# Kernel tuning notes

Hardware: AMD Instinct MI355X
Metric: run time of the kernel (lower is better)

## Reference

```python
import jax, jax.numpy as jnp
import numpy as np


def setup_inputs() -> dict:
    key = jax.random.key(0)
    k1, k2 = jax.random.split(key)
    B, F = 256, 512
    mu_in = jax.random.normal(k1, (B, F), dtype=jnp.float32)
    Sigma_in = jax.random.normal(k2, (B, F, F), dtype=jnp.float32)
    return {"mu_in": mu_in, "Sigma_in": Sigma_in}


def reference(mu_in, Sigma_in):
    # mu_out = softmax(mu_in, axis=1)
    p = jax.nn.softmax(mu_in, axis=1)  # [B, F]
    # Per-sample softmax Jacobian J = diag(p) - p p^T (closed form of the
    # autograd.functional.jacobian block-diagonal the torch code extracts).
    # Sigma_out = J @ Sigma_in @ J^T, computed without materializing J:
    #   (Sigma J^T)_ij = p_j * (Sigma_ij - (Sigma @ p)_i)
    Sp = jnp.einsum("bij,bj->bi", Sigma_in, p)  # [B, F]
    M = p[:, None, :] * (Sigma_in - Sp[:, :, None])  # Sigma @ J^T, [B, F, F]
    #   (J M)_ik = p_i * (M_ik - (p^T M)_k)
    pM = jnp.einsum("bi,bik->bk", p, M)  # [B, F]
    Sigma_out = p[:, :, None] * (M - pM[:, None, :])  # [B, F, F]
    return (p, Sigma_out)
```

## Files before the change

kernel.cpp:

```cpp
#include <hip/hip_runtime.h>

#define FDIM 512
#define CHUNK 32
#define NCH 16

#define WAITVM4() asm volatile("s_waitcnt vmcnt(4)" ::: "memory")
#define WAITVM0() asm volatile("s_waitcnt vmcnt(0)" ::: "memory")
#define WAITLGKM0() asm volatile("s_waitcnt lgkmcnt(0)" ::: "memory")
#define BAR() __builtin_amdgcn_s_barrier()

__device__ __forceinline__ void gld_lds16(const float* g, float* l) {
    __builtin_amdgcn_global_load_lds(
        (const __attribute__((address_space(1))) void*)g,
        (__attribute__((address_space(3))) void*)l, 16, 0, 0);
}

__device__ __forceinline__ void stage_chunk(const float* Sb, int ch, float* buf,
                                            int w, int l) {
    const float* g = Sb + (size_t)(ch * CHUNK + w * 2) * FDIM + l * 4;
    float* d = buf + (w * 2) * FDIM;
    gld_lds16(g,       d);
    gld_lds16(g + 256, d + 256);
    gld_lds16(g + 512, d + 512);
    gld_lds16(g + 768, d + 768);
}

__global__ __launch_bounds__(1024, 1)
void rvsoftmax_fused(const float* __restrict__ mu,
                     const float* __restrict__ Sigma,
                     float* __restrict__ p_out,
                     float* __restrict__ S_out) {
    const int b = blockIdx.x;
    const int t = threadIdx.x;
    const int w = t >> 6;
    const int l = t & 63;

    __shared__ __align__(16) float bufA[CHUNK * FDIM];
    __shared__ __align__(16) float bufB[CHUNK * FDIM];
    __shared__ __align__(16) float p_lds[FDIM];
    __shared__ __align__(16) float r_lds[FDIM];
    __shared__ __align__(16) float c_lds[FDIM];
    __shared__ float red[16];
    __shared__ float sc[2];

    const float* Sb = Sigma + (size_t)b * FDIM * FDIM;

    stage_chunk(Sb, 0, bufA, w, l);

    float x = (t < FDIM) ? mu[(size_t)b * FDIM + t] : -__builtin_inff();
    float m = x;
    #pragma unroll
    for (int off = 32; off >= 1; off >>= 1) m = fmaxf(m, __shfl_xor(m, off));
    if (l == 0) red[w] = m;
    __syncthreads();
    if (t == 0) {
        float mm = red[0];
        for (int j = 1; j < 16; ++j) mm = fmaxf(mm, red[j]);
        sc[0] = mm;
    }
    __syncthreads();
    const float mx = sc[0];
    float e = (t < FDIM) ? __expf(x - mx) : 0.f;
    float ssum = e;
    #pragma unroll
    for (int off = 32; off >= 1; off >>= 1) ssum += __shfl_xor(ssum, off);
    if (l == 0) red[w] = ssum;
    __syncthreads();
    if (t == 0) {
        float tt = 0.f;
        for (int j = 0; j < 16; ++j) tt += red[j];
        sc[0] = tt;
    }
    __syncthreads();
    const float inv = 1.0f / sc[0];
    if (t < FDIM) {
        float pv = e * inv;
        p_lds[t] = pv;
        p_out[(size_t)b * FDIM + t] = pv;
    }
    __syncthreads();

    const float4 p0 = *(const float4*)&p_lds[4 * l];
    const float4 p1 = *(const float4*)&p_lds[256 + 4 * l];

    float4 c0 = make_float4(0.f, 0.f, 0.f, 0.f);
    float4 c1 = make_float4(0.f, 0.f, 0.f, 0.f);

    for (int ch = 0; ch < NCH; ++ch) {
        float* cur = (ch & 1) ? bufB : bufA;
        float* nxt = (ch & 1) ? bufA : bufB;
        if (ch + 1 < NCH) {
            stage_chunk(Sb, ch + 1, nxt, w, l);
            WAITVM4();
        } else {
            WAITVM0();
        }
        BAR();

        #pragma unroll
        for (int q = 0; q < 2; ++q) {
            const int i = ch * CHUNK + w * 2 + q;
            const float* row = cur + (w * 2 + q) * FDIM;
            const float4 a0 = *(const float4*)&row[4 * l];
            const float4 a1 = *(const float4*)&row[256 + 4 * l];
            const float pi = p_lds[i];
            float dot = a0.x * p0.x + a0.y * p0.y + a0.z * p0.z + a0.w * p0.w
                      + a1.x * p1.x + a1.y * p1.y + a1.z * p1.z + a1.w * p1.w;
            #pragma unroll
            for (int off = 32; off >= 1; off >>= 1) dot += __shfl_xor(dot, off);
            if (l == 0) r_lds[i] = dot;
            c0.x += pi * a0.x; c0.y += pi * a0.y; c0.z += pi * a0.z; c0.w += pi * a0.w;
            c1.x += pi * a1.x; c1.y += pi * a1.y; c1.z += pi * a1.z; c1.w += pi * a1.w;
        }
        WAITLGKM0();
        BAR();
    }

    *(float4*)&bufA[w * FDIM + 4 * l] = c0;
    *(float4*)&bufA[w * FDIM + 256 + 4 * l] = c1;
    __syncthreads();
    if (t < FDIM) {
        float cc = 0.f;
        #pragma unroll
        for (int j = 0; j < 16; ++j) cc += bufA[j * FDIM + t];
        c_lds[t] = cc;
    }
    float sv = (t < FDIM) ? p_lds[t] * r_lds[t] : 0.f;
    #pragma unroll
    for (int off = 32; off >= 1; off >>= 1) sv += __shfl_xor(sv, off);
    if (l == 0) red[w] = sv;
    __syncthreads();
    if (t == 0) {
        float tt = 0.f;
        for (int j = 0; j < 16; ++j) tt += red[j];
        sc[1] = tt;
    }
    __syncthreads();
    const float s = sc[1];
    const float4 cc0 = *(const float4*)&c_lds[4 * l];
    const float4 cc1 = *(const float4*)&c_lds[256 + 4 * l];

    float* Ob = S_out + (size_t)b * FDIM * FDIM;

    stage_chunk(Sb, NCH - 1, bufA, w, l);
    for (int it = 0; it < NCH; ++it) {
        const int ch = NCH - 1 - it;
        float* cur = (it & 1) ? bufB : bufA;
        float* nxt = (it & 1) ? bufA : bufB;
        if (it + 1 < NCH) stage_chunk(Sb, ch - 1, nxt, w, l);
        WAITVM4();
        BAR();

        #pragma unroll
        for (int q = 0; q < 2; ++q) {
            const int i = ch * CHUNK + w * 2 + q;
            const float* row = cur + (w * 2 + q) * FDIM;
            const float4 a0 = *(const float4*)&row[4 * l];
            const float4 a1 = *(const float4*)&row[256 + 4 * l];
            const float pi = p_lds[i];
            const float f = s - r_lds[i];
            float4 o0, o1;
            o0.x = pi * p0.x * (a0.x + (f - cc0.x));
            o0.y = pi * p0.y * (a0.y + (f - cc0.y));
            o0.z = pi * p0.z * (a0.z + (f - cc0.z));
            o0.w = pi * p0.w * (a0.w + (f - cc0.w));
            o1.x = pi * p1.x * (a1.x + (f - cc1.x));
            o1.y = pi * p1.y * (a1.y + (f - cc1.y));
            o1.z = pi * p1.z * (a1.z + (f - cc1.z));
            o1.w = pi * p1.w * (a1.w + (f - cc1.w));
            float* orow = Ob + (size_t)i * FDIM;
            *(float4*)&orow[4 * l] = o0;
            *(float4*)&orow[256 + 4 * l] = o1;
        }
        WAITLGKM0();
        BAR();
    }
}

extern "C" void kernel_launch(void* const* d_in, const int* in_sizes, int n_in,
                              void* d_out, int out_size, void* d_ws, size_t ws_size,
                              hipStream_t stream) {
    const float* mu    = (const float*)d_in[0];
    const float* Sigma = (const float*)d_in[1];
    float* p_out = (float*)d_out;
    float* S_out = (float*)d_out + (size_t)256 * 512;
    hipLaunchKernelGGL(rvsoftmax_fused, dim3(256), dim3(1024), 0, stream,
                       mu, Sigma, p_out, S_out);
}
```

Measured before the change: 145.1 us.

## Split fused kernel into three kernels with many more blocks per sample

Replaces the single 256-block fused kernel with three launches, used when the workspace is large enough. The first computes softmax plus per-row dot products and partial column sums over 2048 blocks. The second reduces the partials and the scalar. The third writes the output over 4096 blocks in reverse block order, so the most recently read Sigma slabs may still be in L2/LLC. The aim is to fill more CUs than one block per sample allows, at the cost of reading Sigma twice, extra launches, workspace traffic, and the softmax being recomputed in 8 blocks per sample.

```diff
diff --git a/kernel.cpp b/kernel.cpp
--- a/kernel.cpp
+++ b/kernel.cpp
@@ -1,9 +1,182 @@
 #include <hip/hip_runtime.h>
 
 #define FDIM 512
+
+#define R_OFF      0
+#define C_OFF      131072
+#define S_OFF      262144
+#define CP_OFF     262400
+#define WS_FLOATS  (262400 + 256*8*512)
+
+__device__ __forceinline__ float4 ld4(const float* p) { return *(const float4*)p; }
+
+__global__ __launch_bounds__(512)
+void k2_rc(const float* __restrict__ mu,
+           const float* __restrict__ Sigma,
+           float* __restrict__ p_out,
+           float* __restrict__ ws) {
+    const int bid  = blockIdx.x;
+    const int b    = bid >> 3;
+    const int slab = bid & 7;
+    const int t = threadIdx.x;
+    const int w = t >> 6;
+    const int l = t & 63;
+
+    __shared__ __align__(16) float p_lds[FDIM];
+    __shared__ __align__(16) float cred[8][FDIM];
+    __shared__ float red[8];
+    __shared__ float sc[1];
+
+    float x = mu[(size_t)b * FDIM + t];
+    float m = x;
+    #pragma unroll
+    for (int off = 32; off >= 1; off >>= 1) m = fmaxf(m, __shfl_xor(m, off));
+    if (l == 0) red[w] = m;
+    __syncthreads();
+    if (t == 0) {
+        float mm = red[0];
+        for (int j = 1; j < 8; ++j) mm = fmaxf(mm, red[j]);
+        sc[0] = mm;
+    }
+    __syncthreads();
+    const float mx = sc[0];
+    float e = __expf(x - mx);
+    float ssum = e;
+    #pragma unroll
+    for (int off = 32; off >= 1; off >>= 1) ssum += __shfl_xor(ssum, off);
+    if (l == 0) red[w] = ssum;
+    __syncthreads();
+    if (t == 0) {
+        float tt = 0.f;
+        for (int j = 0; j < 8; ++j) tt += red[j];
+        sc[0] = tt;
+    }
+    __syncthreads();
+    const float pv = e / sc[0];
+    p_lds[t] = pv;
+    if (slab == 0) p_out[(size_t)b * FDIM + t] = pv;
+    __syncthreads();
+
+    const float4 p0 = ld4(&p_lds[4 * l]);
+    const float4 p1 = ld4(&p_lds[256 + 4 * l]);
+
+    const int i0 = slab * 64 + w * 8;
+    const float* rowp = Sigma + (size_t)b * FDIM * FDIM + (size_t)i0 * FDIM + 4 * l;
+    float* r_ws = ws + R_OFF + (size_t)b * FDIM;
+
+    float4 c0 = make_float4(0.f, 0.f, 0.f, 0.f);
+    float4 c1 = make_float4(0.f, 0.f, 0.f, 0.f);
+
+    float4 a0 = ld4(rowp);
+    float4 a1 = ld4(rowp + 256);
+    #pragma unroll
+    for (int q = 0; q < 8; ++q) {
+        float4 n0, n1;
+        if (q < 7) { n0 = ld4(rowp + (q + 1) * FDIM); n1 = ld4(rowp + (q + 1) * FDIM + 256); }
+        const int i = i0 + q;
+        const float pi = p_lds[i];
+        float dot = a0.x * p0.x + a0.y * p0.y + a0.z * p0.z + a0.w * p0.w
+                  + a1.x * p1.x + a1.y * p1.y + a1.z * p1.z + a1.w * p1.w;
+        #pragma unroll
+        for (int off = 32; off >= 1; off >>= 1) dot += __shfl_xor(dot, off);
+        if (l == 0) r_ws[i] = dot;
+        c0.x += pi * a0.x; c0.y += pi * a0.y; c0.z += pi * a0.z; c0.w += pi * a0.w;
+        c1.x += pi * a1.x; c1.y += pi * a1.y; c1.z += pi * a1.z; c1.w += pi * a1.w;
+        if (q < 7) { a0 = n0; a1 = n1; }
+    }
+
+    *(float4*)&cred[w][4 * l] = c0;
+    *(float4*)&cred[w][256 + 4 * l] = c1;
+    __syncthreads();
+    float cc = 0.f;
+    #pragma unroll
+    for (int j = 0; j < 8; ++j) cc += cred[j][t];
+    ws[CP_OFF + ((size_t)b * 8 + slab) * FDIM + t] = cc;
+}
+
+__global__ __launch_bounds__(512)
+void k2b_cs(const float* __restrict__ p_out, float* __restrict__ ws) {
+    const int b = blockIdx.x;
+    const int t = threadIdx.x;
+    const int w = t >> 6;
+    const int l = t & 63;
+    __shared__ float red[8];
+
+    float cc = 0.f;
+    #pragma unroll
+    for (int j = 0; j < 8; ++j)
+        cc += ws[CP_OFF + ((size_t)b * 8 + j) * FDIM + t];
+    ws[C_OFF + (size_t)b * FDIM + t] = cc;
+
+    float sv = p_out[(size_t)b * FDIM + t] * ws[R_OFF + (size_t)b * FDIM + t];
+    #pragma unroll
+    for (int off = 32; off >= 1; off >>= 1) sv += __shfl_xor(sv, off);
+    if (l == 0) red[w] = sv;
+    __syncthreads();
+    if (t == 0) {
+        float tt = 0.f;
+        for (int j = 0; j < 8; ++j) tt += red[j];
+        ws[S_OFF + b] = tt;
+    }
+}
+
+__global__ __launch_bounds__(256)
+void k3_out(const float* __restrict__ Sigma,
+            const float* __restrict__ p_out,
+            const float* __restrict__ ws,
+            float* __restrict__ S_out) {
+    const int bid  = (int)gridDim.x - 1 - (int)blockIdx.x;
+    const int b    = bid >> 4;
+    const int slab = bid & 15;
+    const int t = threadIdx.x;
+    const int w = t >> 6;
+    const int l = t & 63;
+
+    const float* pb = p_out + (size_t)b * FDIM;
+    const float* cb = ws + C_OFF + (size_t)b * FDIM;
+    const float* rb = ws + R_OFF + (size_t)b * FDIM;
+    const float  s  = ws[S_OFF + b];
+
+    const float4 p0 = ld4(&pb[4 * l]);
+    const float4 p1 = ld4(&pb[256 + 4 * l]);
+    const float4 c0 = ld4(&cb[4 * l]);
+    const float4 c1 = ld4(&cb[256 + 4 * l]);
+
+    const int i0 = slab * 32 + w * 8;
+    const float* rowp = Sigma + (size_t)b * FDIM * FDIM + (size_t)i0 * FDIM + 4 * l;
+    float* orow       = S_out + (size_t)b * FDIM * FDIM + (size_t)i0 * FDIM + 4 * l;
+
+    float4 a0 = ld4(rowp);
+    float4 a1 = ld4(rowp + 256);
+    float pi = pb[i0];
+    float ri = rb[i0];
+    #pragma unroll
+    for (int q = 0; q < 8; ++q) {
+        float4 n0, n1; float npi, nri;
+        if (q < 7) {
+            n0 = ld4(rowp + (q + 1) * FDIM);
+            n1 = ld4(rowp + (q + 1) * FDIM + 256);
+            npi = pb[i0 + q + 1];
+            nri = rb[i0 + q + 1];
+        }
+        const float f = s - ri;
+        float4 o0, o1;
+        o0.x = pi * p0.x * (a0.x + (f - c0.x));
+        o0.y = pi * p0.y * (a0.y + (f - c0.y));
+        o0.z = pi * p0.z * (a0.z + (f - c0.z));
+        o0.w = pi * p0.w * (a0.w + (f - c0.w));
+        o1.x = pi * p1.x * (a1.x + (f - c1.x));
+        o1.y = pi * p1.y * (a1.y + (f - c1.y));
+        o1.z = pi * p1.z * (a1.z + (f - c1.z));
+        o1.w = pi * p1.w * (a1.w + (f - c1.w));
+        *(float4*)(orow + q * FDIM) = o0;
+        *(float4*)(orow + q * FDIM + 256) = o1;
+        if (q < 7) { a0 = n0; a1 = n1; pi = npi; ri = nri; }
+    }
+}
+
 #define CHUNK 32
 #define NCH 16
-
 #define WAITVM4() asm volatile("s_waitcnt vmcnt(4)" ::: "memory")
 #define WAITVM0() asm volatile("s_waitcnt vmcnt(0)" ::: "memory")
 #define WAITLGKM0() asm volatile("s_waitcnt lgkmcnt(0)" ::: "memory")
@@ -14,50 +187,33 @@
         (const __attribute__((address_space(1))) void*)g,
         (__attribute__((address_space(3))) void*)l, 16, 0, 0);
 }
-
 __device__ __forceinline__ void stage_chunk(const float* Sb, int ch, float* buf,
                                             int w, int l) {
     const float* g = Sb + (size_t)(ch * CHUNK + w * 2) * FDIM + l * 4;
     float* d = buf + (w * 2) * FDIM;
-    gld_lds16(g,       d);
-    gld_lds16(g + 256, d + 256);
-    gld_lds16(g + 512, d + 512);
-    gld_lds16(g + 768, d + 768);
+    gld_lds16(g, d); gld_lds16(g + 256, d + 256);
+    gld_lds16(g + 512, d + 512); gld_lds16(g + 768, d + 768);
 }
 
 __global__ __launch_bounds__(1024, 1)
-void rvsoftmax_fused(const float* __restrict__ mu,
-                     const float* __restrict__ Sigma,
-                     float* __restrict__ p_out,
-                     float* __restrict__ S_out) {
-    const int b = blockIdx.x;
-    const int t = threadIdx.x;
-    const int w = t >> 6;
-    const int l = t & 63;
-
+void rvsoftmax_fused(const float* __restrict__ mu, const float* __restrict__ Sigma,
+                     float* __restrict__ p_out, float* __restrict__ S_out) {
+    const int b = blockIdx.x, t = threadIdx.x, w = t >> 6, l = t & 63;
     __shared__ __align__(16) float bufA[CHUNK * FDIM];
     __shared__ __align__(16) float bufB[CHUNK * FDIM];
     __shared__ __align__(16) float p_lds[FDIM];
     __shared__ __align__(16) float r_lds[FDIM];
     __shared__ __align__(16) float c_lds[FDIM];
-    __shared__ float red[16];
-    __shared__ float sc[2];
-
+    __shared__ float red[16]; __shared__ float sc[2];
     const float* Sb = Sigma + (size_t)b * FDIM * FDIM;
-
     stage_chunk(Sb, 0, bufA, w, l);
-
     float x = (t < FDIM) ? mu[(size_t)b * FDIM + t] : -__builtin_inff();
     float m = x;
     #pragma unroll
     for (int off = 32; off >= 1; off >>= 1) m = fmaxf(m, __shfl_xor(m, off));
     if (l == 0) red[w] = m;
     __syncthreads();
-    if (t == 0) {
-        float mm = red[0];
-        for (int j = 1; j < 16; ++j) mm = fmaxf(mm, red[j]);
-        sc[0] = mm;
-    }
+    if (t == 0) { float mm = red[0]; for (int j = 1; j < 16; ++j) mm = fmaxf(mm, red[j]); sc[0] = mm; }
     __syncthreads();
     const float mx = sc[0];
     float e = (t < FDIM) ? __expf(x - mx) : 0.f;
@@ -66,43 +222,24 @@
     for (int off = 32; off >= 1; off >>= 1) ssum += __shfl_xor(ssum, off);
     if (l == 0) red[w] = ssum;
     __syncthreads();
-    if (t == 0) {
-        float tt = 0.f;
-        for (int j = 0; j < 16; ++j) tt += red[j];
-        sc[0] = tt;
-    }
+    if (t == 0) { float tt = 0.f; for (int j = 0; j < 16; ++j) tt += red[j]; sc[0] = tt; }
     __syncthreads();
     const float inv = 1.0f / sc[0];
-    if (t < FDIM) {
-        float pv = e * inv;
-        p_lds[t] = pv;
-        p_out[(size_t)b * FDIM + t] = pv;
-    }
-    __syncthreads();
-
-    const float4 p0 = *(const float4*)&p_lds[4 * l];
-    const float4 p1 = *(const float4*)&p_lds[256 + 4 * l];
-
-    float4 c0 = make_float4(0.f, 0.f, 0.f, 0.f);
-    float4 c1 = make_float4(0.f, 0.f, 0.f, 0.f);
-
+    if (t < FDIM) { float pv = e * inv; p_lds[t] = pv; p_out[(size_t)b * FDIM + t] = pv; }
+    __syncthreads();
+    const float4 p0 = ld4(&p_lds[4 * l]);
+    const float4 p1 = ld4(&p_lds[256 + 4 * l]);
+    float4 c0 = make_float4(0.f, 0.f, 0.f, 0.f), c1 = make_float4(0.f, 0.f, 0.f, 0.f);
     for (int ch = 0; ch < NCH; ++ch) {
         float* cur = (ch & 1) ? bufB : bufA;
         float* nxt = (ch & 1) ? bufA : bufB;
-        if (ch + 1 < NCH) {
-            stage_chunk(Sb, ch + 1, nxt, w, l);
-            WAITVM4();
-        } else {
-            WAITVM0();
-        }
+        if (ch + 1 < NCH) { stage_chunk(Sb, ch + 1, nxt, w, l); WAITVM4(); } else { WAITVM0(); }
         BAR();
-
         #pragma unroll
         for (int q = 0; q < 2; ++q) {
             const int i = ch * CHUNK + w * 2 + q;
             const float* row = cur + (w * 2 + q) * FDIM;
-            const float4 a0 = *(const float4*)&row[4 * l];
-            const float4 a1 = *(const float4*)&row[256 + 4 * l];
+            const float4 a0 = ld4(&row[4 * l]); const float4 a1 = ld4(&row[256 + 4 * l]);
             const float pi = p_lds[i];
             float dot = a0.x * p0.x + a0.y * p0.y + a0.z * p0.z + a0.w * p0.w
                       + a1.x * p1.x + a1.y * p1.y + a1.z * p1.z + a1.w * p1.w;
@@ -112,10 +249,8 @@
             c0.x += pi * a0.x; c0.y += pi * a0.y; c0.z += pi * a0.z; c0.w += pi * a0.w;
             c1.x += pi * a1.x; c1.y += pi * a1.y; c1.z += pi * a1.z; c1.w += pi * a1.w;
         }
-        WAITLGKM0();
-        BAR();
-    }
-
+        WAITLGKM0(); BAR();
+    }
     *(float4*)&bufA[w * FDIM + 4 * l] = c0;
     *(float4*)&bufA[w * FDIM + 256 + 4 * l] = c1;
     __syncthreads();
@@ -130,51 +265,36 @@
     for (int off = 32; off >= 1; off >>= 1) sv += __shfl_xor(sv, off);
     if (l == 0) red[w] = sv;
     __syncthreads();
-    if (t == 0) {
-        float tt = 0.f;
-        for (int j = 0; j < 16; ++j) tt += red[j];
-        sc[1] = tt;
-    }
+    if (t == 0) { float tt = 0.f; for (int j = 0; j < 16; ++j) tt += red[j]; sc[1] = tt; }
     __syncthreads();
     const float s = sc[1];
-    const float4 cc0 = *(const float4*)&c_lds[4 * l];
-    const float4 cc1 = *(const float4*)&c_lds[256 + 4 * l];
-
+    const float4 cc0 = ld4(&c_lds[4 * l]); const float4 cc1 = ld4(&c_lds[256 + 4 * l]);
     float* Ob = S_out + (size_t)b * FDIM * FDIM;
-
     stage_chunk(Sb, NCH - 1, bufA, w, l);
     for (int it = 0; it < NCH; ++it) {
         const int ch = NCH - 1 - it;
         float* cur = (it & 1) ? bufB : bufA;
         float* nxt = (it & 1) ? bufA : bufB;
         if (it + 1 < NCH) stage_chunk(Sb, ch - 1, nxt, w, l);
-        WAITVM4();
-        BAR();
-
+        WAITVM4(); BAR();
         #pragma unroll
         for (int q = 0; q < 2; ++q) {
             const int i = ch * CHUNK + w * 2 + q;
             const float* row = cur + (w * 2 + q) * FDIM;
-            const float4 a0 = *(const float4*)&row[4 * l];
-            const float4 a1 = *(const float4*)&row[256 + 4 * l];
+            const float4 a0 = ld4(&row[4 * l]); const float4 a1 = ld4(&row[256 + 4 * l]);
             const float pi = p_lds[i];
             const float f = s - r_lds[i];
             float4 o0, o1;
-            o0.x = pi * p0.x * (a0.x + (f - cc0.x));
-            o0.y = pi * p0.y * (a0.y + (f - cc0.y));
-            o0.z = pi * p0.z * (a0.z + (f - cc0.z));
-            o0.w = pi * p0.w * (a0.w + (f - cc0.w));
-            o1.x = pi * p1.x * (a1.x + (f - cc1.x));
-            o1.y = pi * p1.y * (a1.y + (f - cc1.y));
-            o1.z = pi * p1.z * (a1.z + (f - cc1.z));
-            o1.w = pi * p1.w * (a1.w + (f - cc1.w));
-            float* orow = Ob + (size_t)i * FDIM;
-            *(float4*)&orow[4 * l] = o0;
-            *(float4*)&orow[256 + 4 * l] = o1;
+            o0.x = pi * p0.x * (a0.x + (f - cc0.x)); o0.y = pi * p0.y * (a0.y + (f - cc0.y));
+            o0.z = pi * p0.z * (a0.z + (f - cc0.z)); o0.w = pi * p0.w * (a0.w + (f - cc0.w));
+            o1.x = pi * p1.x * (a1.x + (f - cc1.x)); o1.y = pi * p1.y * (a1.y + (f - cc1.y));
+            o1.z = pi * p1.z * (a1.z + (f - cc1.z)); o1.w = pi * p1.w * (a1.w + (f - cc1.w));
+            float* orow = S_out + (size_t)b * FDIM * FDIM + (size_t)i * FDIM;
+            *(float4*)&orow[4 * l] = o0; *(float4*)&orow[256 + 4 * l] = o1;
         }
-        WAITLGKM0();
-        BAR();
-    }
+        WAITLGKM0(); BAR();
+    }
+    (void)Ob;
 }
 
 extern "C" void kernel_launch(void* const* d_in, const int* in_sizes, int n_in,
@@ -184,6 +304,14 @@
     const float* Sigma = (const float*)d_in[1];
     float* p_out = (float*)d_out;
     float* S_out = (float*)d_out + (size_t)256 * 512;
-    hipLaunchKernelGGL(rvsoftmax_fused, dim3(256), dim3(1024), 0, stream,
-                       mu, Sigma, p_out, S_out);
-}
+
+    if (ws_size >= (size_t)WS_FLOATS * sizeof(float)) {
+        float* ws = (float*)d_ws;
+        hipLaunchKernelGGL(k2_rc,  dim3(2048), dim3(512), 0, stream, mu, Sigma, p_out, ws);
+        hipLaunchKernelGGL(k2b_cs, dim3(256),  dim3(512), 0, stream, p_out, ws);
+        hipLaunchKernelGGL(k3_out, dim3(4096), dim3(256), 0, stream, Sigma, p_out, ws, S_out);
+    } else {
+        hipLaunchKernelGGL(rvsoftmax_fused, dim3(256), dim3(1024), 0, stream,
+                           mu, Sigma, p_out, S_out);
+    }
+}
```

New measurement: 155.3 us. +7.0%, slower.
